# Kernel optimization log

Measured on AMD Instinct MI355X. Metric: run time of the kernel, lower is better.

Reference implementation:

```python
import jax, jax.numpy as jnp
import numpy as np

S, B, H = 512, 256, 500


def setup_inputs() -> dict:
    key = jax.random.key(0)
    k1, k2, k3, k4, k5 = jax.random.split(key, 5)
    return {
        "hidden": jax.random.normal(k1, (1, B, H), dtype=jnp.float32),
        "encoder_output": jax.random.normal(k2, (S, B, H), dtype=jnp.float32),
        "W_attn": jax.random.normal(k3, (H, 2 * H), dtype=jnp.float32) * 0.02,
        "b_attn": jax.random.normal(k4, (H,), dtype=jnp.float32) * 0.02,
        "v": jax.random.normal(k5, (H,), dtype=jnp.float32),
    }


def reference(hidden, encoder_output, W_attn, b_attn, v):
    # hidden: [1, B, H] -> broadcast to [S, B, H]; concat -> [S, B, 2H]
    s, b, h = encoder_output.shape
    h_exp = jnp.broadcast_to(hidden, (s, b, h))
    cat = jnp.concatenate([h_exp, encoder_output], axis=2)  # [S, B, 2H]
    # Linear(2H -> H) with torch convention W: [out, in], then tanh
    energy = jnp.tanh(jnp.einsum("sbi,hi->sbh", cat, W_attn) + b_attn)  # [S, B, H]
    scores = jnp.einsum("sbh,h->sb", energy, v)  # [S, B]
    attn = jax.nn.softmax(scores.T, axis=1)  # [B, S]
    return attn[:, None, :]  # [B, 1, S]
```

## Files before the change

### kernel.cpp

```cpp
#include <hip/hip_runtime.h>
#include <hip/hip_fp16.h>

#define S_DIM 512
#define B_DIM 256
#define H_DIM 500
#define HP    512
#define M_DIM (S_DIM * B_DIM)

typedef _Float16 half8_t __attribute__((ext_vector_type(8)));
typedef float    f32x4  __attribute__((ext_vector_type(4)));

#define WS_W2R 0
#define WS_AT  (512 * 1024)
#define WS_VP  (1024 * 1024)
#define WS_SC  (1024 * 1024 + 4096)

__global__ void prep_w2_v(const float* __restrict__ W, const float* __restrict__ v,
                          _Float16* __restrict__ W2r, float* __restrict__ vp) {
    int idx = blockIdx.x * blockDim.x + threadIdx.x;
#pragma unroll
    for (int r = 0; r < 2; ++r) {
        int e = idx + r * 131072;
        int n = e >> 9, k = e & 511;
        float val = (n < H_DIM && k < H_DIM) ? W[n * 1000 + 500 + k] : 0.0f;
        int dst = ((n >> 4) * 64 + (k >> 3)) * 128 + (n & 15) * 8 + (k & 7);
        W2r[dst] = (_Float16)val;
    }
    if (idx < HP) vp[idx] = (idx < H_DIM) ? v[idx] : 0.0f;
}

__global__ void prep_A(const float* __restrict__ hidden, const float* __restrict__ W,
                       const float* __restrict__ b_attn, float* __restrict__ At) {
    int b = blockIdx.x;
    int t = threadIdx.x;
    __shared__ float hs[HP];
    hs[t] = (t < H_DIM) ? hidden[b * H_DIM + t] : 0.0f;
    __syncthreads();
    float acc = 0.0f;
    if (t < H_DIM) {
        acc = b_attn[t];
        const float4* wr = (const float4*)(W + t * 1000);
        const float4* hr = (const float4*)hs;
#pragma unroll 5
        for (int i = 0; i < 125; ++i) {
            float4 w4 = wr[i], h4 = hr[i];
            acc += w4.x * h4.x + w4.y * h4.y + w4.z * h4.z + w4.w * h4.w;
        }
    }
    At[t * B_DIM + b] = acc;
}

__launch_bounds__(256, 2)
__global__ void fused_attn_gemm(const float* __restrict__ enc,
                                const _Float16* __restrict__ W2r,
                                const float* __restrict__ At,
                                const float* __restrict__ vp,
                                float* __restrict__ sct) {
    __shared__ _Float16 As[2][128][32];
    __shared__ float    red[2][128];

    const int tid  = threadIdx.x;
    const int lane = tid & 63;
    const int wid  = tid >> 6;
    const int wm   = wid >> 1;
    const int wn   = wid & 1;
    const int l15  = lane & 15;
    const int lq   = lane >> 4;

    const int mblk = blockIdx.x;
    const int m0   = mblk * 128;
    const int bloc = (mblk & 1) * 128;
    const int s_idx = mblk >> 1;

    const int r0  = tid >> 2;
    const int r1  = r0 + 64;
    const int cst = tid & 3;
    const float* gA0 = enc + (size_t)(m0 + r0) * H_DIM + cst * 8;
    const float* gA1 = enc + (size_t)(m0 + r1) * H_DIM + cst * 8;
    const int ca0 = (cst ^ ((r0 >> 1) & 3)) * 8;
    const int ca1 = (cst ^ ((r1 >> 1) & 3)) * 8;

    const int rch = (lq ^ ((l15 >> 1) & 3)) * 8;

    const _Float16* gB = W2r + wn * 32768 + lq * 128 + l15 * 8;

    f32x4 a00, a01, a10, a11;
    auto ldA = [&](int kk) {
        if (kk != 480) {
            a00 = *(const f32x4*)(gA0 + kk); a01 = *(const f32x4*)(gA0 + kk + 4);
            a10 = *(const f32x4*)(gA1 + kk); a11 = *(const f32x4*)(gA1 + kk + 4);
        } else {
#pragma unroll
            for (int u = 0; u < 4; ++u) {
                int k = kk + cst * 8 + u;
                a00[u] = (k < H_DIM) ? gA0[kk + u] : 0.0f;
                a10[u] = (k < H_DIM) ? gA1[kk + u] : 0.0f;
                int k2 = k + 4;
                a01[u] = (k2 < H_DIM) ? gA0[kk + 4 + u] : 0.0f;
                a11[u] = (k2 < H_DIM) ? gA1[kk + 4 + u] : 0.0f;
            }
        }
    };
    auto wrA = [&](int buf) {
        half8_t h0, h1;
#pragma unroll
        for (int u = 0; u < 4; ++u) {
            h0[u] = (_Float16)a00[u]; h0[u + 4] = (_Float16)a01[u];
            h1[u] = (_Float16)a10[u]; h1[u + 4] = (_Float16)a11[u];
        }
        *(half8_t*)&As[buf][r0][ca0] = h0;
        *(half8_t*)&As[buf][r1][ca1] = h1;
    };

    float pj[4][4];
#pragma unroll
    for (int mf = 0; mf < 4; ++mf)
#pragma unroll
        for (int j = 0; j < 4; ++j) pj[mf][j] = 0.0f;

    for (int nc = 0; nc < 4; ++nc) {
        f32x4 acc[4][4];
#pragma unroll
        for (int a = 0; a < 4; ++a)
#pragma unroll
            for (int b = 0; b < 4; ++b) acc[a][b] = 0;

        ldA(0);
        wrA(0);

#pragma unroll
        for (int ks = 0; ks < 16; ++ks) {
            __syncthreads();
            if (ks < 15) ldA((ks + 1) * 32);

            half8_t bfc[4];
#pragma unroll
            for (int nf = 0; nf < 4; ++nf)
                bfc[nf] = *(const half8_t*)(gB + nc * 65536 + nf * 8192 + ks * 512);

            half8_t af[4];
#pragma unroll
            for (int mf = 0; mf < 4; ++mf)
                af[mf] = *(const half8_t*)&As[ks & 1][wm * 64 + mf * 16 + l15][rch];

#pragma unroll
            for (int mf = 0; mf < 4; ++mf)
#pragma unroll
                for (int nf = 0; nf < 4; ++nf)
                    acc[mf][nf] = __builtin_amdgcn_mfma_f32_16x16x32_f16(af[mf], bfc[nf], acc[mf][nf], 0, 0, 0);

            if (ks < 15) wrA((ks & 1) ^ 1);
        }

        float vpv[4];
#pragma unroll
        for (int nf = 0; nf < 4; ++nf) vpv[nf] = vp[nc * 128 + wn * 64 + nf * 16 + l15];

#pragma unroll
        for (int mf = 0; mf < 4; ++mf) {
#pragma unroll
            for (int nf = 0; nf < 4; ++nf) {
                int h = nc * 128 + wn * 64 + nf * 16 + l15;
                f32x4 av = *(const f32x4*)(At + h * B_DIM + bloc + wm * 64 + mf * 16 + lq * 4);
#pragma unroll
                for (int j = 0; j < 4; ++j) {
                    float x  = acc[mf][nf][j] + av[j];
                    float xc = fminf(fmaxf(x, -9.0f), 9.0f);
                    float e  = __expf(2.0f * xc);
                    float th = (e - 1.0f) / (e + 1.0f);
                    pj[mf][j] += vpv[nf] * th;
                }
            }
        }
    }

#pragma unroll
    for (int mf = 0; mf < 4; ++mf)
#pragma unroll
        for (int j = 0; j < 4; ++j) {
            float s = pj[mf][j];
            s += __shfl_xor(s, 1); s += __shfl_xor(s, 2);
            s += __shfl_xor(s, 4); s += __shfl_xor(s, 8);
            if (l15 == 0) red[wn][wm * 64 + mf * 16 + lq * 4 + j] = s;
        }
    __syncthreads();
    if (tid < 128) {
        float p = red[0][tid] + red[1][tid];
        sct[(size_t)(bloc + tid) * S_DIM + s_idx] = p;
    }
}

__global__ void softmax_rows(const float* __restrict__ sct, float* __restrict__ out) {
    int b = blockIdx.x;
    int t = threadIdx.x;
    int lane = t & 63, w = t >> 6;
    float v = sct[(size_t)b * S_DIM + t];
    float m = v;
#pragma unroll
    for (int off = 1; off < 64; off <<= 1) m = fmaxf(m, __shfl_xor(m, off));
    __shared__ float sm[8], ss[8];
    if (lane == 0) sm[w] = m;
    __syncthreads();
    m = sm[0];
#pragma unroll
    for (int i = 1; i < 8; ++i) m = fmaxf(m, sm[i]);
    float e = __expf(v - m);
    float s = e;
#pragma unroll
    for (int off = 1; off < 64; off <<= 1) s += __shfl_xor(s, off);
    if (lane == 0) ss[w] = s;
    __syncthreads();
    s = ss[0];
#pragma unroll
    for (int i = 1; i < 8; ++i) s += ss[i];
    out[(size_t)b * S_DIM + t] = e / s;
}

extern "C" void kernel_launch(void* const* d_in, const int* in_sizes, int n_in,
                              void* d_out, int out_size, void* d_ws, size_t ws_size,
                              hipStream_t stream) {
    const float* hidden = (const float*)d_in[0];
    const float* enc    = (const float*)d_in[1];
    const float* W      = (const float*)d_in[2];
    const float* b_attn = (const float*)d_in[3];
    const float* v      = (const float*)d_in[4];
    float* out = (float*)d_out;

    char* ws = (char*)d_ws;
    _Float16* W2r = (_Float16*)(ws + WS_W2R);
    float*    At  = (float*)(ws + WS_AT);
    float*    vp  = (float*)(ws + WS_VP);
    float*    sct = (float*)(ws + WS_SC);

    prep_w2_v<<<512, 256, 0, stream>>>(W, v, W2r, vp);
    prep_A<<<256, 512, 0, stream>>>(hidden, W, b_attn, At);
    fused_attn_gemm<<<1024, 256, 0, stream>>>(enc, W2r, At, vp, sct);
    softmax_rows<<<256, 512, 0, stream>>>(sct, out);
}
```

Measured before the change: 226.0 us.

## Stage full-K encoder tile in LDS once and split N across eight waves

The fused GEMM kernel now loads a 64-row by full-K encoder tile into shared memory once, converting it to fp16, and drops the double-buffered 32-wide K pipeline that was re-read for each of four N chunks. Each of eight waves covers a distinct 64-column slice of H, so the encoder data is read from global once per block instead of four times, and the per-k-step barriers go away. The costs are a larger LDS footprint (about 66KB per block), no overlap between global loads and MFMA work, and W2 fragments still fetched from global by every wave.

```diff
diff --git a/kernel.cpp b/kernel.cpp
--- a/kernel.cpp
+++ b/kernel.cpp
@@ -4,7 +4,6 @@
 #define S_DIM 512
 #define B_DIM 256
 #define H_DIM 500
-#define HP    512
 #define M_DIM (S_DIM * B_DIM)
 
 typedef _Float16 half8_t __attribute__((ext_vector_type(8)));
@@ -26,14 +25,14 @@
         int dst = ((n >> 4) * 64 + (k >> 3)) * 128 + (n & 15) * 8 + (k & 7);
         W2r[dst] = (_Float16)val;
     }
-    if (idx < HP) vp[idx] = (idx < H_DIM) ? v[idx] : 0.0f;
+    if (idx < 512) vp[idx] = (idx < H_DIM) ? v[idx] : 0.0f;
 }
 
 __global__ void prep_A(const float* __restrict__ hidden, const float* __restrict__ W,
                        const float* __restrict__ b_attn, float* __restrict__ At) {
     int b = blockIdx.x;
     int t = threadIdx.x;
-    __shared__ float hs[HP];
+    __shared__ float hs[512];
     hs[t] = (t < H_DIM) ? hidden[b * H_DIM + t] : 0.0f;
     __syncthreads();
     float acc = 0.0f;
@@ -50,67 +49,75 @@
     At[t * B_DIM + b] = acc;
 }
 
-__launch_bounds__(256, 2)
+__launch_bounds__(512, 4)
 __global__ void fused_attn_gemm(const float* __restrict__ enc,
                                 const _Float16* __restrict__ W2r,
                                 const float* __restrict__ At,
                                 const float* __restrict__ vp,
                                 float* __restrict__ sct) {
-    __shared__ _Float16 As[2][128][32];
-    __shared__ float    red[2][128];
+    __shared__ _Float16 As[64][520];
+    __shared__ float    red[8][64];
 
     const int tid  = threadIdx.x;
     const int lane = tid & 63;
     const int wid  = tid >> 6;
-    const int wm   = wid >> 1;
-    const int wn   = wid & 1;
     const int l15  = lane & 15;
     const int lq   = lane >> 4;
 
-    const int mblk = blockIdx.x;
-    const int m0   = mblk * 128;
-    const int bloc = (mblk & 1) * 128;
-    const int s_idx = mblk >> 1;
-
-    const int r0  = tid >> 2;
-    const int r1  = r0 + 64;
-    const int cst = tid & 3;
-    const float* gA0 = enc + (size_t)(m0 + r0) * H_DIM + cst * 8;
-    const float* gA1 = enc + (size_t)(m0 + r1) * H_DIM + cst * 8;
-    const int ca0 = (cst ^ ((r0 >> 1) & 3)) * 8;
-    const int ca1 = (cst ^ ((r1 >> 1) & 3)) * 8;
-
-    const int rch = (lq ^ ((l15 >> 1) & 3)) * 8;
-
-    const _Float16* gB = W2r + wn * 32768 + lq * 128 + l15 * 8;
-
-    f32x4 a00, a01, a10, a11;
-    auto ldA = [&](int kk) {
-        if (kk != 480) {
-            a00 = *(const f32x4*)(gA0 + kk); a01 = *(const f32x4*)(gA0 + kk + 4);
-            a10 = *(const f32x4*)(gA1 + kk); a11 = *(const f32x4*)(gA1 + kk + 4);
-        } else {
-#pragma unroll
-            for (int u = 0; u < 4; ++u) {
-                int k = kk + cst * 8 + u;
-                a00[u] = (k < H_DIM) ? gA0[kk + u] : 0.0f;
-                a10[u] = (k < H_DIM) ? gA1[kk + u] : 0.0f;
-                int k2 = k + 4;
-                a01[u] = (k2 < H_DIM) ? gA0[kk + 4 + u] : 0.0f;
-                a11[u] = (k2 < H_DIM) ? gA1[kk + 4 + u] : 0.0f;
+    const int mblk  = blockIdx.x;
+    const int m0    = mblk * 64;
+    const int s_idx = mblk >> 2;
+    const int bbase = (mblk & 3) * 64;
+
+    {
+        const int r  = tid >> 3;
+        const int jc = tid & 7;
+        const float* gr = enc + (size_t)(m0 + r) * H_DIM;
+#pragma unroll
+        for (int i = 0; i < 8; ++i) {
+            int c = jc + i * 8;
+            f32x4 v0 = {0, 0, 0, 0}, v1 = {0, 0, 0, 0};
+            if (c < 62) {
+                v0 = *(const f32x4*)(gr + c * 8);
+                v1 = *(const f32x4*)(gr + c * 8 + 4);
+            } else if (c == 62) {
+                v0 = *(const f32x4*)(gr + 496);
             }
-        }
-    };
-    auto wrA = [&](int buf) {
-        half8_t h0, h1;
-#pragma unroll
-        for (int u = 0; u < 4; ++u) {
-            h0[u] = (_Float16)a00[u]; h0[u + 4] = (_Float16)a01[u];
-            h1[u] = (_Float16)a10[u]; h1[u + 4] = (_Float16)a11[u];
-        }
-        *(half8_t*)&As[buf][r0][ca0] = h0;
-        *(half8_t*)&As[buf][r1][ca1] = h1;
-    };
+            half8_t h;
+#pragma unroll
+            for (int u = 0; u < 4; ++u) { h[u] = (_Float16)v0[u]; h[u + 4] = (_Float16)v1[u]; }
+            *(half8_t*)&As[r][c * 8] = h;
+        }
+    }
+    __syncthreads();
+
+    const _Float16* gB = W2r + (size_t)wid * 32768 + lq * 128 + l15 * 8;
+
+    f32x4 acc[4][4];
+#pragma unroll
+    for (int a = 0; a < 4; ++a)
+#pragma unroll
+        for (int b = 0; b < 4; ++b) acc[a][b] = 0;
+
+#pragma unroll 2
+    for (int ks = 0; ks < 16; ++ks) {
+        half8_t bq[4], af[4];
+#pragma unroll
+        for (int nf = 0; nf < 4; ++nf)
+            bq[nf] = *(const half8_t*)(gB + nf * 8192 + ks * 512);
+#pragma unroll
+        for (int mf = 0; mf < 4; ++mf)
+            af[mf] = *(const half8_t*)&As[mf * 16 + l15][(ks * 4 + lq) * 8];
+#pragma unroll
+        for (int nf = 0; nf < 4; ++nf)
+#pragma unroll
+            for (int mf = 0; mf < 4; ++mf)
+                acc[mf][nf] = __builtin_amdgcn_mfma_f32_16x16x32_f16(af[mf], bq[nf], acc[mf][nf], 0, 0, 0);
+    }
+
+    float vpv[4];
+#pragma unroll
+    for (int nf = 0; nf < 4; ++nf) vpv[nf] = vp[wid * 64 + nf * 16 + l15];
 
     float pj[4][4];
 #pragma unroll
@@ -118,58 +125,19 @@
 #pragma unroll
         for (int j = 0; j < 4; ++j) pj[mf][j] = 0.0f;
 
-    for (int nc = 0; nc < 4; ++nc) {
-        f32x4 acc[4][4];
-#pragma unroll
-        for (int a = 0; a < 4; ++a)
-#pragma unroll
-            for (int b = 0; b < 4; ++b) acc[a][b] = 0;
-
-        ldA(0);
-        wrA(0);
-
-#pragma unroll
-        for (int ks = 0; ks < 16; ++ks) {
-            __syncthreads();
-            if (ks < 15) ldA((ks + 1) * 32);
-
-            half8_t bfc[4];
-#pragma unroll
-            for (int nf = 0; nf < 4; ++nf)
-                bfc[nf] = *(const half8_t*)(gB + nc * 65536 + nf * 8192 + ks * 512);
-
-            half8_t af[4];
-#pragma unroll
-            for (int mf = 0; mf < 4; ++mf)
-                af[mf] = *(const half8_t*)&As[ks & 1][wm * 64 + mf * 16 + l15][rch];
-
-#pragma unroll
-            for (int mf = 0; mf < 4; ++mf)
-#pragma unroll
-                for (int nf = 0; nf < 4; ++nf)
-                    acc[mf][nf] = __builtin_amdgcn_mfma_f32_16x16x32_f16(af[mf], bfc[nf], acc[mf][nf], 0, 0, 0);
-
-            if (ks < 15) wrA((ks & 1) ^ 1);
-        }
-
-        float vpv[4];
-#pragma unroll
-        for (int nf = 0; nf < 4; ++nf) vpv[nf] = vp[nc * 128 + wn * 64 + nf * 16 + l15];
-
-#pragma unroll
-        for (int mf = 0; mf < 4; ++mf) {
-#pragma unroll
-            for (int nf = 0; nf < 4; ++nf) {
-                int h = nc * 128 + wn * 64 + nf * 16 + l15;
-                f32x4 av = *(const f32x4*)(At + h * B_DIM + bloc + wm * 64 + mf * 16 + lq * 4);
-#pragma unroll
-                for (int j = 0; j < 4; ++j) {
-                    float x  = acc[mf][nf][j] + av[j];
-                    float xc = fminf(fmaxf(x, -9.0f), 9.0f);
-                    float e  = __expf(2.0f * xc);
-                    float th = (e - 1.0f) / (e + 1.0f);
-                    pj[mf][j] += vpv[nf] * th;
-                }
+#pragma unroll
+    for (int mf = 0; mf < 4; ++mf) {
+#pragma unroll
+        for (int nf = 0; nf < 4; ++nf) {
+            int h = wid * 64 + nf * 16 + l15;
+            f32x4 av = *(const f32x4*)(At + h * B_DIM + bbase + mf * 16 + lq * 4);
+#pragma unroll
+            for (int j = 0; j < 4; ++j) {
+                float x  = acc[mf][nf][j] + av[j];
+                float xc = fminf(fmaxf(x, -9.0f), 9.0f);
+                float e  = __expf(2.0f * xc);
+                float th = (e - 1.0f) / (e + 1.0f);
+                pj[mf][j] += vpv[nf] * th;
             }
         }
     }
@@ -181,12 +149,14 @@
             float s = pj[mf][j];
             s += __shfl_xor(s, 1); s += __shfl_xor(s, 2);
             s += __shfl_xor(s, 4); s += __shfl_xor(s, 8);
-            if (l15 == 0) red[wn][wm * 64 + mf * 16 + lq * 4 + j] = s;
-        }
-    __syncthreads();
-    if (tid < 128) {
-        float p = red[0][tid] + red[1][tid];
-        sct[(size_t)(bloc + tid) * S_DIM + s_idx] = p;
+            if (l15 == 0) red[wid][mf * 16 + lq * 4 + j] = s;
+        }
+    __syncthreads();
+    if (tid < 64) {
+        float p = 0.0f;
+#pragma unroll
+        for (int w = 0; w < 8; ++w) p += red[w][tid];
+        sct[(size_t)(bbase + tid) * S_DIM + s_idx] = p;
     }
 }
 
@@ -234,6 +204,6 @@
 
     prep_w2_v<<<512, 256, 0, stream>>>(W, v, W2r, vp);
     prep_A<<<256, 512, 0, stream>>>(hidden, W, b_attn, At);
-    fused_attn_gemm<<<1024, 256, 0, stream>>>(enc, W2r, At, vp, sct);
+    fused_attn_gemm<<<2048, 512, 0, stream>>>(enc, W2r, At, vp, sct);
     softmax_rows<<<256, 512, 0, stream>>>(sct, out);
 }
```

Result: faster. 208.8 us (-7.6%).
